# Performance work log

Hardware: AMD Instinct MI355X
Metric: run time of the kernel (lower is better)

The kernel has to match this reference:

```python
import jax, jax.numpy as jnp
import numpy as np

K = 5          # top_k periods
KERNEL = 25    # moving-average kernel for series decomposition
D = 64         # d_model / channels
EPS = 1e-5     # BatchNorm eps (torch default)


def setup_inputs() -> dict:
    key = jax.random.key(0)
    k0, k1, k2, k3, k4 = jax.random.split(key, 5)
    B, T = 8, 2048
    x = jax.random.normal(k0, (B, T, D), jnp.float32)
    w1 = jax.random.normal(k1, (D, D, 3, 3), jnp.float32) * 0.05
    w2 = jax.random.normal(k2, (D, D, 3, 3), jnp.float32) * 0.05
    bn1_gamma = jnp.ones((D,), jnp.float32) + 0.1 * jax.random.normal(k3, (D,), jnp.float32)
    bn2_gamma = jnp.ones((D,), jnp.float32) + 0.1 * jax.random.normal(k4, (D,), jnp.float32)
    z = jnp.zeros((D,), jnp.float32)
    o = jnp.ones((D,), jnp.float32)
    return dict(x=x, w1=w1, w2=w2,
                bn1_gamma=bn1_gamma, bn1_beta=z, bn1_mean=z, bn1_var=o,
                bn2_gamma=bn2_gamma, bn2_beta=z, bn2_mean=z, bn2_var=o)


def _moving_avg(x, kernel):
    # AvgPool1d(stride=1, padding=(kernel-1)//2, count_include_pad=False) over time.
    T = x.shape[1]
    pad = (kernel - 1) // 2
    cs = jnp.concatenate([jnp.zeros_like(x[:, :1]), jnp.cumsum(x, axis=1)], axis=1)  # [B,T+1,C]
    t = jnp.arange(T)
    lo = jnp.clip(t - pad, 0, T)          # inclusive window start
    hi = jnp.clip(t + pad + 1, 0, T)      # exclusive window end
    sums = cs[:, hi] - cs[:, lo]
    return sums / (hi - lo).astype(x.dtype)[None, :, None]


def _auto_corr(s, k):
    T = s.shape[1]
    Xf = jnp.fft.rfft(s, axis=1)
    Pm = (Xf * jnp.conj(Xf)).real.mean(axis=-1)          # [B, T//2+1]
    r = jnp.fft.irfft(Pm, n=T, axis=1)                   # [B, T]
    r = r.at[:, 0].set(-jnp.inf)                          # forbid lag 0
    vals, idx = jax.lax.top_k(r, k)                       # [B,k]
    w = jax.nn.softmax(vals, axis=1)
    return idx, w


def _bn(z, gamma, beta, mean, var):
    return (z - mean) * (gamma * jax.lax.rsqrt(var + EPS)) + beta


def _process_one(s_b, p, w1, w2, bn1, bn2):
    # s_b: [T, C]; p: scalar int period.
    # Equivalent to: roll(s_b, -p), reflect-pad time to cyc*p, fold to [C,cyc,p],
    # Conv2dResBlock (3x3 zero-pad convs + eval BN + GELU + residual), unfold, crop to T.
    T, C = s_b.shape
    U = 2 * T - 2                               # static bound: cyc*p <= T+p-1 <= 2T-2
    u = jnp.arange(U)
    cyc = (T + p - 1) // p
    v = jnp.where(u < T, u, 2 * T - 2 - u)      # reflect extension index
    g = s_b[(v + p) % T]                         # [U,C] rolled-by-(-p) then reflect-padded
    r = u // p                                   # grid row (cycle)
    c = u % p                                    # grid col (phase)

    def conv3x3(z, w):
        # zero-padded 3x3 conv on the [cyc, p] grid, expressed on the flat time axis
        out = jnp.zeros_like(z)
        for dr in (-1, 0, 1):
            for dc in (-1, 0, 1):
                valid = (r + dr >= 0) & (r + dr < cyc) & (c + dc >= 0) & (c + dc < p)
                un = jnp.clip(u + dr * p + dc, 0, U - 1)
                zn = jnp.where(valid[:, None], z[un], 0.0)    # [U,C]
                out = out + zn @ w[:, :, dr + 1, dc + 1].T    # [U,Cout]
        return out

    h = _bn(conv3x3(g, w1), *bn1)
    h = jax.nn.gelu(h, approximate=False)
    h = _bn(conv3x3(h, w2), *bn2)
    return (g + h)[:T]                           # residual + unfold-crop


def reference(x, w1, w2, bn1_gamma, bn1_beta, bn1_mean, bn1_var,
              bn2_gamma, bn2_beta, bn2_mean, bn2_var):
    trend = _moving_avg(x, KERNEL)
    s = x - trend                                # seasonal
    idx, w = _auto_corr(s, K)                    # [B,K] periods, weights
    bn1 = (bn1_gamma, bn1_beta, bn1_mean, bn1_var)
    bn2 = (bn2_gamma, bn2_beta, bn2_mean, bn2_var)
    f = lambda sb, p: _process_one(sb, p, w1, w2, bn1, bn2)
    y = jax.vmap(lambda sb, pb: jax.vmap(lambda p: f(sb, p))(pb))(s, idx)  # [B,K,T,C]
    agg = jnp.einsum('bk,bktc->btc', w, y)
    return agg + trend + x
```

## Files before the change

### kernel.cpp

```cpp
#include <hip/hip_runtime.h>
#include <hip/hip_bf16.h>
#include <math.h>

#define TB 8
#define TT 2048
#define TD 64
#define TK 5
#define TPAD 12
#define EPSBN 1e-5f
#define UMAX 4096

#define ROWS 64
#define BAND 66
#define LROWS 198

typedef __attribute__((ext_vector_type(8))) short short8;
typedef __attribute__((ext_vector_type(4))) float f32x4;

#define OFF_S     0
#define OFF_SBF   1048576
#define OFF_R     1572864
#define OFF_IDX   1581056
#define OFF_W     1581096
#define OFF_WT1   1581136
#define OFF_WT2   1599568
#define OFF_H1    1618000

__global__ __launch_bounds__(256) void k_trend(const float* __restrict__ x,
                                               float* __restrict__ out, float* __restrict__ s,
                                               __hip_bfloat16* __restrict__ sbf,
                                               const float* __restrict__ w1, const float* __restrict__ w2,
                                               __hip_bfloat16* __restrict__ wt1, __hip_bfloat16* __restrict__ wt2)
{
    if (blockIdx.x >= 256) {
        int d = (blockIdx.x - 256) * 256 + threadIdx.x;
        if (d < 36864) {
            int j = d & 7, l = (d >> 3) & 63, nt = (d >> 9) & 3, kb = d >> 11;
            int tap = kb >> 1, half = kb & 1;
            int co = nt * 16 + (l & 15);
            int ci = half * 32 + (l >> 4) * 8 + j;
            int src = (co * 64 + ci) * 9 + tap;
            wt1[d] = __float2bfloat16(w1[src]);
            wt2[d] = __float2bfloat16(w2[src]);
        }
        return;
    }
    int gid = blockIdx.x * 256 + threadIdx.x;
    int c = gid & 63;
    int tblk = (gid >> 6) & 127;
    int b = gid >> 13;
    int t0 = tblk * 16;
    const float* base = x + (size_t)b * TT * TD + c;
    float sum = 0.f;
    for (int tt = t0 - TPAD; tt <= t0 + TPAD; ++tt)
        if (tt >= 0 && tt < TT) sum += base[(size_t)tt * TD];
    size_t o = (size_t)b * TT * TD + (size_t)t0 * TD + c;
    #pragma unroll
    for (int i = 0; i < 16; ++i) {
        int t = t0 + i;
        int lo = t - TPAD; if (lo < 0) lo = 0;
        int hi = t + TPAD; if (hi > TT - 1) hi = TT - 1;
        float tr = sum / (float)(hi - lo + 1);
        float xv = base[(size_t)t * TD];
        out[o] = xv + tr;
        float sv = xv - tr;
        s[o] = sv;
        sbf[o] = __float2bfloat16(sv);
        int addt = t + TPAD + 1, subt = t - TPAD;
        if (addt < TT) sum += base[(size_t)addt * TD];
        if (subt >= 0) sum -= base[(size_t)subt * TD];
        o += TD;
    }
}

__global__ __launch_bounds__(256) void k_autocorr(const float* __restrict__ s, float* __restrict__ r)
{
    int b = blockIdx.z;
    int l0 = blockIdx.x * 16 + 1;
    const float* sb = s + (size_t)b * TT * TD;
    int cg = (threadIdx.x & 15) * 4;
    int tg = threadIdx.x >> 4;
    int t0 = blockIdx.y * 1024 + tg * 64;
    const int RB = TD * 4;
    const int TTB = TT * TD * 4;
    float acc[16];
    #pragma unroll
    for (int j = 0; j < 16; ++j) acc[j] = 0.f;
    float4 win[16];
    int wi = t0 + l0; if (wi >= TT) wi -= TT;
    int woff = wi * RB + cg * 4;
    int aoff = t0 * RB + cg * 4;
    #pragma unroll
    for (int m = 0; m < 16; ++m) {
        win[m] = *(const float4*)((const char*)sb + woff);
        woff += RB; if (woff >= TTB) woff -= TTB;
    }
    for (int it = 0; it < 4; ++it) {
        #pragma unroll
        for (int jj = 0; jj < 16; ++jj) {
            float4 a = *(const float4*)((const char*)sb + aoff);
            aoff += RB;
            #pragma unroll
            for (int j = 0; j < 16; ++j) {
                float4 w = win[(jj + j) & 15];
                acc[j] = fmaf(a.x, w.x, acc[j]);
                acc[j] = fmaf(a.y, w.y, acc[j]);
                acc[j] = fmaf(a.z, w.z, acc[j]);
                acc[j] = fmaf(a.w, w.w, acc[j]);
            }
            win[jj] = *(const float4*)((const char*)sb + woff);
            woff += RB; if (woff >= TTB) woff -= TTB;
        }
    }
    __shared__ float red[16 * 256];
    #pragma unroll
    for (int j = 0; j < 16; ++j) red[j * 256 + threadIdx.x] = acc[j];
    __syncthreads();
    int j = threadIdx.x >> 4, i = threadIdx.x & 15;
    float v = 0.f;
    #pragma unroll
    for (int m = 0; m < 16; ++m) v += red[j * 256 + i + 16 * m];
    #pragma unroll
    for (int mask = 8; mask; mask >>= 1) v += __shfl_xor(v, mask);
    if (i == 0) atomicAdd(&r[(size_t)b * 1024 + (l0 - 1 + j)], v * (1.0f / 64.0f));
}

__global__ __launch_bounds__(256) void k_topk(const float* __restrict__ r,
                                              int* __restrict__ selidx, float* __restrict__ selw)
{
    int b = blockIdx.x;
    __shared__ float v[1024];
    __shared__ float redv[256]; __shared__ int redi[256];
    __shared__ int s_idx[6]; __shared__ float s_val[6]; __shared__ int slots;
    for (int i = threadIdx.x; i < 1024; i += 256) v[i] = r[(size_t)b * 1024 + i];
    if (threadIdx.x == 0) slots = 0;
    __syncthreads();
    for (int round = 0; round < 5; ++round) {
        if (slots >= 5) break;
        float bv = -INFINITY; int bi = 1 << 30;
        for (int i = threadIdx.x; i < 1024; i += 256) {
            float val = v[i];
            if (val > bv) { bv = val; bi = i; }
        }
        redv[threadIdx.x] = bv; redi[threadIdx.x] = bi;
        __syncthreads();
        for (int off = 128; off; off >>= 1) {
            if (threadIdx.x < off) {
                float ov = redv[threadIdx.x + off]; int oi = redi[threadIdx.x + off];
                float mv = redv[threadIdx.x];       int mi = redi[threadIdx.x];
                if (ov > mv || (ov == mv && oi < mi)) { redv[threadIdx.x] = ov; redi[threadIdx.x] = oi; }
            }
            __syncthreads();
        }
        if (threadIdx.x == 0) {
            int lag = redi[0] + 1; float val = redv[0];
            s_idx[slots] = lag; s_val[slots] = val; slots++;
            if (slots < 5 && lag < 1024) { s_idx[slots] = 2048 - lag; s_val[slots] = val; slots++; }
            v[lag - 1] = -INFINITY;
        }
        __syncthreads();
    }
    if (threadIdx.x == 0) {
        float mx = -INFINITY;
        for (int i = 0; i < 5; ++i) mx = fmaxf(mx, s_val[i]);
        float e[5], sum = 0.f;
        for (int i = 0; i < 5; ++i) { e[i] = expf(s_val[i] - mx); sum += e[i]; }
        for (int i = 0; i < 5; ++i) { selidx[b * TK + i] = s_idx[i]; selw[b * TK + i] = e[i] / sum; }
    }
}

__global__ __launch_bounds__(128) void k_mm1(
    const short* __restrict__ s_bf, const short* __restrict__ wtp,
    const float* __restrict__ g1, const float* __restrict__ b1,
    const float* __restrict__ m1, const float* __restrict__ v1,
    const int* __restrict__ sel, __hip_bfloat16* __restrict__ h1)
{
    int b = blockIdx.z, k = blockIdx.y;
    int p = sel[b * TK + k];
    int cyc = (TT + p - 1) / p;
    int U = cyc * p;
    int u0 = blockIdx.x * ROWS;
    if (u0 >= U) return;
    __shared__ short As[LROWS * 64];

    const short* sb = s_bf + (size_t)b * TT * TD;
    for (int q = threadIdx.x; q < LROWS * 8; q += 128) {
        int row = q >> 3, ch = (q & 7) * 8;
        int band = row / BAND, i = row - band * BAND;
        int w = u0 + (band - 1) * p - 1 + i;
        int wc = min(max(w, 0), 2 * TT - 2);
        int v = (wc < TT) ? wc : (2 * TT - 2 - wc);
        int sr = (v + p) & (TT - 1);
        short8 d = *(const short8*)(sb + (size_t)sr * TD + ch);
        int off = (row * 128 + ch * 2) ^ ((row & 7) << 4);
        *(short8*)((char*)As + off) = d;
    }
    __syncthreads();

    int lane = threadIdx.x & 63;
    int wv = threadIdx.x >> 6;
    int lr = lane & 15;
    int kg = lane >> 4;
    bool inU[2], topf[2], botf[2], leftf[2], rightf[2];
    int lu[2];
    #pragma unroll
    for (int rs = 0; rs < 2; ++rs) {
        lu[rs] = wv * 32 + rs * 16 + lr;
        int u = u0 + lu[rs];
        inU[rs] = (u < U);
        int r = u / p, c = u - r * p;
        topf[rs] = (r == 0); botf[rs] = (r == cyc - 1);
        leftf[rs] = (c == 0); rightf[rs] = (c == p - 1);
    }
    f32x4 acc[2][4] = {};
    short8 zero = {};
    #pragma unroll
    for (int kb = 0; kb < 18; ++kb) {
        const int tap = kb >> 1, half = kb & 1;
        const int dr = tap / 3 - 1, dc = tap % 3 - 1;
        short8 a[2];
        #pragma unroll
        for (int rs = 0; rs < 2; ++rs) {
            int ldsrow = (dr + 1) * BAND + lu[rs] + 1 + dc;
            int off = (ldsrow * 128 + half * 64 + kg * 16) ^ ((ldsrow & 7) << 4);
            a[rs] = *(const short8*)((const char*)As + off);
            bool valid = inU[rs]
                       && !(dr == -1 && topf[rs]) && !(dr == 1 && botf[rs])
                       && !(dc == -1 && leftf[rs]) && !(dc == 1 && rightf[rs]);
            if (!valid) a[rs] = zero;
        }
        #pragma unroll
        for (int nt = 0; nt < 4; ++nt) {
            short8 bq = *(const short8*)(wtp + (size_t)(kb * 4 + nt) * 512 + lane * 8);
            #pragma unroll
            for (int rs = 0; rs < 2; ++rs)
                acc[rs][nt] = __builtin_amdgcn_mfma_f32_16x16x32_bf16(a[rs], bq, acc[rs][nt], 0, 0, 0);
        }
    }
    __hip_bfloat16* ho = h1 + (size_t)(b * TK + k) * (UMAX * TD);
    #pragma unroll
    for (int nt = 0; nt < 4; ++nt) {
        int co = nt * 16 + lr;
        float scale = g1[co] * rsqrtf(v1[co] + EPSBN);
        float bias = b1[co] - m1[co] * scale;
        #pragma unroll
        for (int rs = 0; rs < 2; ++rs) {
            int ub = u0 + wv * 32 + rs * 16 + kg * 4;
            #pragma unroll
            for (int q = 0; q < 4; ++q) {
                int u = ub + q;
                if (u < U) {
                    float z = acc[rs][nt][q] * scale + bias;
                    float ge = 0.5f * z * (1.0f + erff(z * 0.70710678118654752f));
                    ho[(size_t)u * TD + co] = __float2bfloat16(ge);
                }
            }
        }
    }
}

__global__ __launch_bounds__(128) void k_mm2(
    const short* __restrict__ h1, const short* __restrict__ wtp,
    const float* __restrict__ s,
    const float* __restrict__ g2, const float* __restrict__ b2,
    const float* __restrict__ m2, const float* __restrict__ v2,
    const int* __restrict__ sel, const float* __restrict__ selw,
    float* __restrict__ out)
{
    int b = blockIdx.z, k = blockIdx.y;
    int p = sel[b * TK + k];
    float wk = selw[b * TK + k];
    int cyc = (TT + p - 1) / p;
    int u0 = blockIdx.x * ROWS;
    __shared__ short As[LROWS * 64];

    const short* hb = h1 + (size_t)(b * TK + k) * (UMAX * TD);
    for (int q = threadIdx.x; q < LROWS * 8; q += 128) {
        int row = q >> 3, ch = (q & 7) * 8;
        int band = row / BAND, i = row - band * BAND;
        int w = u0 + (band - 1) * p - 1 + i;
        int wc = min(max(w, 0), UMAX - 1);
        short8 d = *(const short8*)(hb + (size_t)wc * TD + ch);
        int off = (row * 128 + ch * 2) ^ ((row & 7) << 4);
        *(short8*)((char*)As + off) = d;
    }
    __syncthreads();

    int lane = threadIdx.x & 63;
    int wv = threadIdx.x >> 6;
    int lr = lane & 15;
    int kg = lane >> 4;
    bool topf[2], botf[2], leftf[2], rightf[2];
    int lu[2];
    #pragma unroll
    for (int rs = 0; rs < 2; ++rs) {
        lu[rs] = wv * 32 + rs * 16 + lr;
        int u = u0 + lu[rs];
        int r = u / p, c = u - r * p;
        topf[rs] = (r == 0); botf[rs] = (r == cyc - 1);
        leftf[rs] = (c == 0); rightf[rs] = (c == p - 1);
    }
    f32x4 acc[2][4] = {};
    short8 zero = {};
    #pragma unroll
    for (int kb = 0; kb < 18; ++kb) {
        const int tap = kb >> 1, half = kb & 1;
        const int dr = tap / 3 - 1, dc = tap % 3 - 1;
        short8 a[2];
        #pragma unroll
        for (int rs = 0; rs < 2; ++rs) {
            int ldsrow = (dr + 1) * BAND + lu[rs] + 1 + dc;
            int off = (ldsrow * 128 + half * 64 + kg * 16) ^ ((ldsrow & 7) << 4);
            a[rs] = *(const short8*)((const char*)As + off);
            bool valid = !(dr == -1 && topf[rs]) && !(dr == 1 && botf[rs])
                       && !(dc == -1 && leftf[rs]) && !(dc == 1 && rightf[rs]);
            if (!valid) a[rs] = zero;
        }
        #pragma unroll
        for (int nt = 0; nt < 4; ++nt) {
            short8 bq = *(const short8*)(wtp + (size_t)(kb * 4 + nt) * 512 + lane * 8);
            #pragma unroll
            for (int rs = 0; rs < 2; ++rs)
                acc[rs][nt] = __builtin_amdgcn_mfma_f32_16x16x32_bf16(a[rs], bq, acc[rs][nt], 0, 0, 0);
        }
    }
    const float* sb = s + (size_t)b * TT * TD;
    float* ob = out + (size_t)b * TT * TD;
    #pragma unroll
    for (int nt = 0; nt < 4; ++nt) {
        int co = nt * 16 + lr;
        float scale = g2[co] * rsqrtf(v2[co] + EPSBN);
        float bias = b2[co] - m2[co] * scale;
        #pragma unroll
        for (int rs = 0; rs < 2; ++rs) {
            int ub = u0 + wv * 32 + rs * 16 + kg * 4;
            #pragma unroll
            for (int q = 0; q < 4; ++q) {
                int u = ub + q;
                int sr = (u + p) & (TT - 1);
                float gval = sb[(size_t)sr * TD + co];
                float z = acc[rs][nt][q] * scale + bias;
                atomicAdd(&ob[(size_t)u * TD + co], wk * (gval + z));
            }
        }
    }
}

extern "C" void kernel_launch(void* const* d_in, const int* in_sizes, int n_in,
                              void* d_out, int out_size, void* d_ws, size_t ws_size,
                              hipStream_t stream)
{
    const float* x  = (const float*)d_in[0];
    const float* w1 = (const float*)d_in[1];
    const float* w2 = (const float*)d_in[2];
    const float* g1 = (const float*)d_in[3];
    const float* b1 = (const float*)d_in[4];
    const float* m1 = (const float*)d_in[5];
    const float* v1 = (const float*)d_in[6];
    const float* g2 = (const float*)d_in[7];
    const float* b2 = (const float*)d_in[8];
    const float* m2 = (const float*)d_in[9];
    const float* v2 = (const float*)d_in[10];

    float* ws    = (float*)d_ws;
    float* s     = ws + OFF_S;
    __hip_bfloat16* sbf = (__hip_bfloat16*)(ws + OFF_SBF);
    float* r     = ws + OFF_R;
    int*   sel   = (int*)(ws + OFF_IDX);
    float* selw  = ws + OFF_W;
    __hip_bfloat16* wt1 = (__hip_bfloat16*)(ws + OFF_WT1);
    __hip_bfloat16* wt2 = (__hip_bfloat16*)(ws + OFF_WT2);
    __hip_bfloat16* h1  = (__hip_bfloat16*)(ws + OFF_H1);
    float* out   = (float*)d_out;

    k_trend   <<<dim3(400),         dim3(256), 0, stream>>>(x, out, s, sbf, w1, w2, wt1, wt2);
    hipMemsetAsync(r, 0, (size_t)TB * 1024 * sizeof(float), stream);
    k_autocorr<<<dim3(64, 2, TB),   dim3(256), 0, stream>>>(s, r);
    k_topk    <<<dim3(TB),          dim3(256), 0, stream>>>(r, sel, selw);
    k_mm1     <<<dim3(64, TK, TB),  dim3(128), 0, stream>>>((const short*)sbf, (const short*)wt1,
                                                            g1, b1, m1, v1, sel, h1);
    k_mm2     <<<dim3(32, TK, TB),  dim3(128), 0, stream>>>((const short*)h1, (const short*)wt2, s,
                                                            g2, b2, m2, v2, sel, selw, out);
}
```

Measured before the change: 136.7 us.

## Fuse top-k period loop into mm2 with double-buffered LDS and no atomics

```diff
diff --git a/kernel.cpp b/kernel.cpp
--- a/kernel.cpp
+++ b/kernel.cpp
@@ -13,6 +13,12 @@
 #define ROWS 64
 #define BAND 66
 #define LROWS 198
+
+#define ROWS2 32
+#define BAND2 34
+#define LROWS2 102
+#define SH8   816
+#define BUFB  13056
 
 typedef __attribute__((ext_vector_type(8))) short short8;
 typedef __attribute__((ext_vector_type(4))) float f32x4;
@@ -259,7 +265,7 @@
     }
 }
 
-__global__ __launch_bounds__(128) void k_mm2(
+__global__ __launch_bounds__(128) void k_mm2f(
     const short* __restrict__ h1, const short* __restrict__ wtp,
     const float* __restrict__ s,
     const float* __restrict__ g2, const float* __restrict__ b2,
@@ -267,64 +273,114 @@
     const int* __restrict__ sel, const float* __restrict__ selw,
     float* __restrict__ out)
 {
-    int b = blockIdx.z, k = blockIdx.y;
-    int p = sel[b * TK + k];
-    float wk = selw[b * TK + k];
-    int cyc = (TT + p - 1) / p;
-    int u0 = blockIdx.x * ROWS;
-    __shared__ short As[LROWS * 64];
-
-    const short* hb = h1 + (size_t)(b * TK + k) * (UMAX * TD);
-    for (int q = threadIdx.x; q < LROWS * 8; q += 128) {
-        int row = q >> 3, ch = (q & 7) * 8;
-        int band = row / BAND, i = row - band * BAND;
-        int w = u0 + (band - 1) * p - 1 + i;
-        int wc = min(max(w, 0), UMAX - 1);
-        short8 d = *(const short8*)(hb + (size_t)wc * TD + ch);
-        int off = (row * 128 + ch * 2) ^ ((row & 7) << 4);
-        *(short8*)((char*)As + off) = d;
+    int b = blockIdx.y;
+    int u0 = blockIdx.x * ROWS2;
+    int tid = threadIdx.x;
+    __shared__ short As[2 * LROWS2 * 64];
+
+    int lane = tid & 63, wv = tid >> 6, lr = lane & 15, kg = lane >> 4;
+    int lu = wv * 16 + lr;
+    int u = u0 + lu;
+    const float* sb = s + (size_t)b * TT * TD;
+
+    f32x4 accT[4] = {};
+    float gacc[4][4] = {};
+    short8 sreg[7];
+    short8 zero = {};
+
+    {
+        int p0 = sel[b * TK];
+        const short* hb = h1 + (size_t)(b * TK) * (UMAX * TD);
+        #pragma unroll
+        for (int it = 0; it < 7; ++it) {
+            int q = tid + it * 128;
+            if (q < SH8) {
+                int row = q >> 3, ch = (q & 7) * 8;
+                int band = row / BAND2, i = row - band * BAND2;
+                int w = u0 + (band - 1) * p0 - 1 + i;
+                int wc = min(max(w, 0), UMAX - 1);
+                sreg[it] = *(const short8*)(hb + (size_t)wc * TD + ch);
+            }
+        }
+        #pragma unroll
+        for (int it = 0; it < 7; ++it) {
+            int q = tid + it * 128;
+            if (q < SH8) {
+                int row = q >> 3, ch = (q & 7) * 8;
+                int off = (row * 128 + ch * 2) ^ ((row & 7) << 4);
+                *(short8*)((char*)As + off) = sreg[it];
+            }
+        }
     }
     __syncthreads();
 
-    int lane = threadIdx.x & 63;
-    int wv = threadIdx.x >> 6;
-    int lr = lane & 15;
-    int kg = lane >> 4;
-    bool topf[2], botf[2], leftf[2], rightf[2];
-    int lu[2];
-    #pragma unroll
-    for (int rs = 0; rs < 2; ++rs) {
-        lu[rs] = wv * 32 + rs * 16 + lr;
-        int u = u0 + lu[rs];
+    for (int k = 0; k < TK; ++k) {
+        int p = sel[b * TK + k];
+        float wk = selw[b * TK + k];
+        int cyc = (TT + p - 1) / p;
+        if (k < TK - 1) {
+            int pn = sel[b * TK + k + 1];
+            const short* hb = h1 + (size_t)(b * TK + k + 1) * (UMAX * TD);
+            #pragma unroll
+            for (int it = 0; it < 7; ++it) {
+                int q = tid + it * 128;
+                if (q < SH8) {
+                    int row = q >> 3, ch = (q & 7) * 8;
+                    int band = row / BAND2, i = row - band * BAND2;
+                    int w = u0 + (band - 1) * pn - 1 + i;
+                    int wc = min(max(w, 0), UMAX - 1);
+                    sreg[it] = *(const short8*)(hb + (size_t)wc * TD + ch);
+                }
+            }
+        }
+        const char* Ab = (const char*)As + (k & 1) * BUFB;
         int r = u / p, c = u - r * p;
-        topf[rs] = (r == 0); botf[rs] = (r == cyc - 1);
-        leftf[rs] = (c == 0); rightf[rs] = (c == p - 1);
-    }
-    f32x4 acc[2][4] = {};
-    short8 zero = {};
-    #pragma unroll
-    for (int kb = 0; kb < 18; ++kb) {
-        const int tap = kb >> 1, half = kb & 1;
-        const int dr = tap / 3 - 1, dc = tap % 3 - 1;
-        short8 a[2];
-        #pragma unroll
-        for (int rs = 0; rs < 2; ++rs) {
-            int ldsrow = (dr + 1) * BAND + lu[rs] + 1 + dc;
+        bool topf = (r == 0), botf = (r == cyc - 1), leftf = (c == 0), rightf = (c == p - 1);
+        f32x4 accP[4] = {};
+        #pragma unroll
+        for (int kb = 0; kb < 18; ++kb) {
+            const int tap = kb >> 1, half = kb & 1;
+            const int dr = tap / 3 - 1, dc = tap % 3 - 1;
+            int ldsrow = (dr + 1) * BAND2 + lu + 1 + dc;
             int off = (ldsrow * 128 + half * 64 + kg * 16) ^ ((ldsrow & 7) << 4);
-            a[rs] = *(const short8*)((const char*)As + off);
-            bool valid = !(dr == -1 && topf[rs]) && !(dr == 1 && botf[rs])
-                       && !(dc == -1 && leftf[rs]) && !(dc == 1 && rightf[rs]);
-            if (!valid) a[rs] = zero;
-        }
-        #pragma unroll
-        for (int nt = 0; nt < 4; ++nt) {
-            short8 bq = *(const short8*)(wtp + (size_t)(kb * 4 + nt) * 512 + lane * 8);
-            #pragma unroll
-            for (int rs = 0; rs < 2; ++rs)
-                acc[rs][nt] = __builtin_amdgcn_mfma_f32_16x16x32_bf16(a[rs], bq, acc[rs][nt], 0, 0, 0);
-        }
-    }
-    const float* sb = s + (size_t)b * TT * TD;
+            short8 a = *(const short8*)(Ab + off);
+            bool valid = !(dr == -1 && topf) && !(dr == 1 && botf)
+                       && !(dc == -1 && leftf) && !(dc == 1 && rightf);
+            if (!valid) a = zero;
+            #pragma unroll
+            for (int nt = 0; nt < 4; ++nt) {
+                short8 bq = *(const short8*)(wtp + (size_t)(kb * 4 + nt) * 512 + lane * 8);
+                accP[nt] = __builtin_amdgcn_mfma_f32_16x16x32_bf16(a, bq, accP[nt], 0, 0, 0);
+            }
+        }
+        #pragma unroll
+        for (int nt = 0; nt < 4; ++nt)
+            #pragma unroll
+            for (int e = 0; e < 4; ++e) accT[nt][e] += wk * accP[nt][e];
+        #pragma unroll
+        for (int q = 0; q < 4; ++q) {
+            int uo = u0 + wv * 16 + kg * 4 + q;
+            int sr = (uo + p) & (TT - 1);
+            #pragma unroll
+            for (int nt = 0; nt < 4; ++nt)
+                gacc[nt][q] = fmaf(wk, sb[(size_t)sr * TD + nt * 16 + lr], gacc[nt][q]);
+        }
+        __syncthreads();
+        if (k < TK - 1) {
+            char* Aw = (char*)As + ((k + 1) & 1) * BUFB;
+            #pragma unroll
+            for (int it = 0; it < 7; ++it) {
+                int q = tid + it * 128;
+                if (q < SH8) {
+                    int row = q >> 3, ch = (q & 7) * 8;
+                    int off = (row * 128 + ch * 2) ^ ((row & 7) << 4);
+                    *(short8*)(Aw + off) = sreg[it];
+                }
+            }
+            __syncthreads();
+        }
+    }
+
     float* ob = out + (size_t)b * TT * TD;
     #pragma unroll
     for (int nt = 0; nt < 4; ++nt) {
@@ -332,16 +388,10 @@
         float scale = g2[co] * rsqrtf(v2[co] + EPSBN);
         float bias = b2[co] - m2[co] * scale;
         #pragma unroll
-        for (int rs = 0; rs < 2; ++rs) {
-            int ub = u0 + wv * 32 + rs * 16 + kg * 4;
-            #pragma unroll
-            for (int q = 0; q < 4; ++q) {
-                int u = ub + q;
-                int sr = (u + p) & (TT - 1);
-                float gval = sb[(size_t)sr * TD + co];
-                float z = acc[rs][nt][q] * scale + bias;
-                atomicAdd(&ob[(size_t)u * TD + co], wk * (gval + z));
-            }
+        for (int q = 0; q < 4; ++q) {
+            int uo = u0 + wv * 16 + kg * 4 + q;
+            size_t idx = (size_t)uo * TD + co;
+            ob[idx] = ob[idx] + gacc[nt][q] + scale * accT[nt][q] + bias;
         }
     }
 }
@@ -379,6 +429,6 @@
     k_topk    <<<dim3(TB),          dim3(256), 0, stream>>>(r, sel, selw);
     k_mm1     <<<dim3(64, TK, TB),  dim3(128), 0, stream>>>((const short*)sbf, (const short*)wt1,
                                                             g1, b1, m1, v1, sel, h1);
-    k_mm2     <<<dim3(32, TK, TB),  dim3(128), 0, stream>>>((const short*)h1, (const short*)wt2, s,
+    k_mm2f    <<<dim3(64, TB),      dim3(128), 0, stream>>>((const short*)h1, (const short*)wt2, s,
                                                             g2, b2, m2, v2, sel, selw, out);
 }
```

After: 142.2 us. 4.0% more time.
